# Kernel tuning notes

Hardware: AMD Instinct MI355X
Metric: run time of the kernel (lower is better)

Reference implementation:

```python
import jax, jax.numpy as jnp
import numpy as np

N = 50000
E = 800000
C_IN = 32
C_OUT = 32
K = 8  # number of branch MLPs


def setup_inputs() -> dict:
    key = jax.random.key(0)
    ks = jax.random.split(key, 12)
    x = jax.random.normal(ks[0], (N, C_IN), dtype=jnp.float32)
    pos = jax.random.normal(ks[1], (N, 2), dtype=jnp.float32)
    edge_index = jax.random.randint(ks[2], (2, E), 0, N, dtype=jnp.int32)
    edge_attr = jax.random.normal(ks[3], (E, 4), dtype=jnp.float32)
    edge_weight = jax.random.uniform(ks[4], (E,), dtype=jnp.float32)
    s1 = 1.0 / np.sqrt(C_IN + 4)
    s2 = 1.0 / np.sqrt(C_OUT)
    W1 = jax.random.uniform(ks[5], (K, C_IN + 4, C_OUT), jnp.float32, -s1, s1)
    b1 = jax.random.uniform(ks[6], (K, C_OUT), jnp.float32, -s1, s1)
    W2 = jax.random.uniform(ks[7], (K, C_OUT, C_OUT), jnp.float32, -s2, s2)
    b2 = jax.random.uniform(ks[8], (K, C_OUT), jnp.float32, -s2, s2)
    sr = 1.0 / np.sqrt(C_IN)
    Wr = jax.random.uniform(ks[9], (C_IN, C_OUT), jnp.float32, -sr, sr)
    br = jax.random.uniform(ks[10], (C_OUT,), jnp.float32, -sr, sr)
    return {"x": x, "pos": pos, "edge_index": edge_index, "edge_attr": edge_attr,
            "edge_weight": edge_weight, "W1": W1, "b1": b1, "W2": W2, "b2": b2,
            "Wr": Wr, "br": br}


def reference(x, pos, edge_index, edge_attr, edge_weight, W1, b1, W2, b2, Wr, br):
    src = edge_index[0]  # j (source / neighbor)
    tgt = edge_index[1]  # i (target / aggregation index)

    # gather per-edge features
    x_i = x[tgt]                      # [E, C_IN]
    x_j = x[src]                      # [E, C_IN]
    diff = pos[src] - pos[tgt]        # [E, 2]

    # geometric branch index in [0, 8)
    con0 = (diff[:, 0] > 0).astype(jnp.int32)
    con1 = (diff[:, 1] > 0).astype(jnp.int32)
    con2 = (jnp.abs(diff[:, 0]) - jnp.abs(diff[:, 1]) > 0).astype(jnp.int32)
    idx = con0 + con1 * 2 + con2 * 4  # [E]

    m = jnp.concatenate([x_j - x_i, edge_attr], axis=1)  # [E, C_IN+4]
    # all 8 branch MLPs (Linear->ReLU->Linear->ReLU), then select per edge
    h = jax.nn.relu(jnp.einsum('ec,kcf->ekf', m, W1) + b1[None])   # [E, K, C_OUT]
    f_all = jax.nn.relu(jnp.einsum('ekf,kfg->ekg', h, W2) + b2[None])
    f = jnp.take_along_axis(f_all, idx[:, None, None], axis=1)[:, 0, :]  # [E, C_OUT]
    f = edge_weight[:, None] * f

    # scatter-mean over target nodes
    seg_sum = jax.ops.segment_sum(f, tgt, num_segments=N)
    counts = jax.ops.segment_sum(jnp.ones((f.shape[0],), f.dtype), tgt, num_segments=N)
    out = seg_sum / jnp.maximum(counts, 1.0)[:, None]

    # skip connection
    out = out + x @ Wr + br
    return out
```

## Files before the change

### kernel.cpp

```cpp
#include <hip/hip_runtime.h>

#define N_NODES 50000
#define N_EDGES 800000
#define K_BR    8
#define BCAP    131072
#define MLP_SLOTS (K_BR * BCAP)
#define SCAN_BLOCKS 196
#define BSTRIDE 1024
#define EPT 8
#define P1_BLOCKS 391
#define RB 128
#define RBE 6250


typedef _Float16 h2 __attribute__((ext_vector_type(2)));
typedef _Float16 half8 __attribute__((ext_vector_type(8)));
typedef float f32x4 __attribute__((ext_vector_type(4)));

#define MFMA(a, b, c) __builtin_amdgcn_mfma_f32_16x16x32_f16((a), (b), (c), 0, 0, 0)

#define VAL_MASK 0x3FFFFFFFu
#define FLG_A    0x40000000u
#define FLG_P    0x80000000u


__device__ __forceinline__ int branch_idx(float dx, float dy) {
    return (dx > 0.0f ? 1 : 0) + (dy > 0.0f ? 2 : 0) +
           ((fabsf(dx) - fabsf(dy)) > 0.0f ? 4 : 0);
}

__device__ __forceinline__ unsigned pk_f16pair(float a, float b) {
    h2 p; p.x = (_Float16)a; p.y = (_Float16)b;
    return __builtin_bit_cast(unsigned, p);
}

__device__ __forceinline__ unsigned short f16bits(float a) {
    _Float16 h = (_Float16)a;
    return __builtin_bit_cast(unsigned short, h);
}

__global__ void __launch_bounds__(256) rank_kernel(
    const int* __restrict__ ei, const float* __restrict__ x,
    const float* __restrict__ W1, const float* __restrict__ W2,
    unsigned short* __restrict__ rankB, unsigned short* __restrict__ cntM,
    unsigned* __restrict__ xh, uint4* __restrict__ w1f4, uint4* __restrict__ w2f4) {
    __shared__ unsigned hist[N_NODES / 2];
    int t = threadIdx.x, b = blockIdx.x;
    for (int i = t; i < N_NODES / 2; i += 256) hist[i] = 0;

    int tid = b * 256 + t;
    if (tid < 2048) {
        int L = tid & 63, fl = tid >> 6;
        int nt = fl & 1, kt = (fl >> 1) & 1, k = fl >> 2;
        int quad = L >> 4, col = L & 15;
        unsigned dw[4];
#pragma unroll
        for (int i = 0; i < 4; ++i) {
            float v0 = 0.0f, v1 = 0.0f;
            int k0 = kt * 32 + quad * 8 + 2 * i;
            if (k0 < 36)     v0 = W1[k * 1152 + k0 * 32 + nt * 16 + col];
            if (k0 + 1 < 36) v1 = W1[k * 1152 + (k0 + 1) * 32 + nt * 16 + col];
            dw[i] = pk_f16pair(v0, v1);
        }
        w1f4[tid] = make_uint4(dw[0], dw[1], dw[2], dw[3]);
    } else if (tid < 3072) {
        int u2 = tid - 2048;
        int L = u2 & 63, fl = u2 >> 6;
        int nt = fl & 1, k = fl >> 1;
        int quad = L >> 4, col = L & 15;
        unsigned dw[4];
#pragma unroll
        for (int i = 0; i < 4; ++i) {
            int k0 = quad * 8 + 2 * i;
            dw[i] = pk_f16pair(W2[k * 1024 + k0 * 32 + nt * 16 + col],
                               W2[k * 1024 + (k0 + 1) * 32 + nt * 16 + col]);
        }
        w2f4[u2] = make_uint4(dw[0], dw[1], dw[2], dw[3]);
    }

    __syncthreads();
    int eb = b * RBE;
    for (int it = 0; it < (RBE + 255) / 256; ++it) {
        int r = it * 256 + t;
        if (r < RBE) {
            int e = eb + r;
            int d = ei[N_EDGES + e];
            unsigned add = (d & 1) ? (1u << 16) : 1u;
            unsigned old = atomicAdd(&hist[d >> 1], add);
            unsigned rk = (d & 1) ? (old >> 16) : (old & 0xFFFFu);
            rankB[e] = (unsigned short)rk;
            float2 xv = ((const float2*)x)[e];
            xh[e] = pk_f16pair(xv.x, xv.y);
        }
    }
    __syncthreads();
    unsigned* cm = (unsigned*)(cntM + (size_t)b * N_NODES);
    for (int i = t; i < N_NODES / 2; i += 256) cm[i] = hist[i];
}

__global__ void colscan_kernel(const unsigned short* __restrict__ cntM,
                               unsigned short* __restrict__ blkBase,
                               int* __restrict__ cnt) {
    int d = blockIdx.x * 256 + threadIdx.x;
    if (d >= N_NODES) return;
    int acc = 0;
#pragma unroll 8
    for (int b = 0; b < RB; ++b) {
        size_t i = (size_t)b * N_NODES + d;
        int v = cntM[i];
        blkBase[i] = (unsigned short)acc;
        acc += v;
    }
    cnt[d] = acc;
}

__global__ void pass1_kernel(const int* __restrict__ ei, const float* __restrict__ pos,
                             const float* __restrict__ ea, const float* __restrict__ ew,
                             const unsigned short* __restrict__ rankB,
                             const unsigned short* __restrict__ blkBase,
                             int* __restrict__ bucketCur,
                             uint4* __restrict__ payload) {
    __shared__ int h[K_BR];
    __shared__ int base[K_BR];
    int t = threadIdx.x;
    if (t < K_BR) h[t] = 0;
    __syncthreads();

    int eBase = blockIdx.x * (256 * EPT);
    int sA[EPT], dA[EPT], krA[EPT], slA[EPT];
#pragma unroll
    for (int it = 0; it < EPT; ++it) {
        int e = eBase + it * 256 + t;
        int s = 0, d = 0, k = 0, rank = 0, slot = 0;
        if (e < N_EDGES) {
            s = ei[e]; d = ei[N_EDGES + e];
            float2 ps2 = ((const float2*)pos)[s];
            float2 pd2 = ((const float2*)pos)[d];
            k = branch_idx(ps2.x - pd2.x, ps2.y - pd2.y);
            rank = atomicAdd(&h[k], 1);
            int bb = e / RBE;
            slot = (int)blkBase[(size_t)bb * N_NODES + d] + (int)rankB[e];
        }
        sA[it] = s; dA[it] = d; krA[it] = (k << 16) | rank; slA[it] = slot;
    }
    __syncthreads();
    if (t < K_BR) base[t] = (h[t] > 0) ? atomicAdd(&bucketCur[t * BSTRIDE], h[t]) : 0;
    __syncthreads();
#pragma unroll
    for (int it = 0; it < EPT; ++it) {
        int e = eBase + it * 256 + t;
        if (e < N_EDGES) {
            int k = krA[it] >> 16, rank = krA[it] & 0xFFFF;
            float4 eav = ((const float4*)ea)[e];
            unsigned ewh = (unsigned)f16bits(ew[e]);
            int idx = (k << 17) + base[k] + rank;
            payload[idx] = make_uint4((unsigned)sA[it] | ((unsigned)dA[it] << 16),
                                      (unsigned)slA[it] | (ewh << 16),
                                      pk_f16pair(eav.x, eav.y),
                                      pk_f16pair(eav.z, eav.w));
        }
    }
}

__global__ void scan_kernel(const int* __restrict__ cnt, unsigned* __restrict__ ps,
                            int* __restrict__ nodeStart) {
    __shared__ int s[256];
    __shared__ int sh_off;
    int t = threadIdx.x, b = blockIdx.x;
    int i = b * 256 + t;
    int v = (i < N_NODES) ? cnt[i] : 0;
    s[t] = v;
    __syncthreads();
#pragma unroll
    for (int off = 1; off < 256; off <<= 1) {
        int tmp = (t >= off) ? s[t - off] : 0;
        __syncthreads();
        s[t] += tmp;
        __syncthreads();
    }
    int excl = s[t] - v;
    if (t == 255)
        atomicExch(&ps[b], (unsigned)s[255] | (b == 0 ? FLG_P : FLG_A));
    if (t == 0) sh_off = 0;
    if (t < 64 && b > 0) {
        int off = 0;
        int base = b - 1;
        for (;;) {
            int idx = base - t;
            unsigned w = 0;
            if (idx >= 0) {
                do { w = atomicOr(&ps[idx], 0u); } while (!(w & (FLG_A | FLG_P)));
            }
            bool isP = (w & FLG_P) != 0;
            unsigned long long pm = __ballot(isP);
            int firstP = pm ? (__ffsll((unsigned long long)pm) - 1) : 64;
            int contrib = (idx >= 0 && t <= firstP) ? (int)(w & VAL_MASK) : 0;
#pragma unroll
            for (int sh = 32; sh > 0; sh >>= 1) contrib += __shfl_down(contrib, sh, 64);
            contrib = __shfl(contrib, 0, 64);
            off += contrib;
            if (firstP < 64 || base - 64 < 0) break;
            base -= 64;
        }
        if (t == 0) sh_off = off;
    }
    __syncthreads();
    if (i < N_NODES) nodeStart[i] = excl + sh_off;
}

__global__ void __launch_bounds__(128, 4) mlp_kernel(
    const uint4* __restrict__ payload,
    const unsigned* __restrict__ xh,
    const uint4* __restrict__ w1f4, const float* __restrict__ b1,
    const uint4* __restrict__ w2f4, const float* __restrict__ b2,
    const int* __restrict__ nodeStart,
    const int* __restrict__ bucketFill,
    unsigned short* __restrict__ fbuf) {
    __shared__ uint4 lds4[164];
    char* hreg = (char*)lds4 + (threadIdx.x >> 6) * 1312;

    int t = blockIdx.x * 128 + threadIdx.x;
    int u = __builtin_amdgcn_readfirstlane(t);
    int k = u >> 17;
    int fill = bucketFill[k * BSTRIDE];
    if ((u & (BCAP - 1)) >= fill) return;
    int rel = t & (BCAP - 1);
    bool valid = rel < fill;
    int idx = (k << 17) + min(rel, fill - 1);

    int L = threadIdx.x & 63;
    int quad = L >> 4, col = L & 15;

    uint4 pl = payload[idx];
    int s = (int)(pl.x & 0xFFFFu);
    int d = (int)(pl.x >> 16);
    float whf = (float)__builtin_bit_cast(_Float16, (unsigned short)(pl.y >> 16));
    int slot = valid ? (nodeStart[d] + (int)(pl.y & 0xFFFFu)) : 0;
    int vld = valid ? 1 : 0;

    half8 B1[2][2], B2[2];
#pragma unroll
    for (int kt = 0; kt < 2; ++kt)
#pragma unroll
        for (int nt = 0; nt < 2; ++nt)
            B1[kt][nt] = __builtin_bit_cast(half8, w1f4[((k * 2 + kt) * 2 + nt) * 64 + L]);
#pragma unroll
    for (int nt = 0; nt < 2; ++nt)
        B2[nt] = __builtin_bit_cast(half8, w2f4[(k * 2 + nt) * 64 + L]);
    float b1o0 = b1[k * 32 + col],      b1o1 = b1[k * 32 + 16 + col];
    float b2o0 = b2[k * 32 + col],      b2o1 = b2[k * 32 + 16 + col];

#pragma unroll
    for (int mt = 0; mt < 4; ++mt) {
        int erA = mt * 16 + col;
        int sA = __shfl(s, erA, 64);
        int dAi = __shfl(d, erA, 64);
        unsigned zA = (unsigned)__shfl((int)pl.z, erA, 64);
        unsigned wA = (unsigned)__shfl((int)pl.w, erA, 64);
        uint4 xjv = ((const uint4*)xh)[4 * (size_t)sA + quad];
        uint4 xiv = ((const uint4*)xh)[4 * (size_t)dAi + quad];
        half8 a0 = __builtin_bit_cast(half8, xjv) - __builtin_bit_cast(half8, xiv);
        uint4 a1u = make_uint4(quad == 0 ? zA : 0u, quad == 0 ? wA : 0u, 0u, 0u);
        half8 a1 = __builtin_bit_cast(half8, a1u);

        f32x4 c0 = {b1o0, b1o0, b1o0, b1o0};
        f32x4 c1 = {b1o1, b1o1, b1o1, b1o1};
        c0 = MFMA(a0, B1[0][0], c0);
        c0 = MFMA(a1, B1[1][0], c0);
        c1 = MFMA(a0, B1[0][1], c1);
        c1 = MFMA(a1, B1[1][1], c1);
#pragma unroll
        for (int r = 0; r < 4; ++r) {
            int er = quad * 4 + r;
            *(unsigned short*)(hreg + er * 80 + col * 2)        = f16bits(fmaxf(c0[r], 0.0f));
            *(unsigned short*)(hreg + er * 80 + (16 + col) * 2) = f16bits(fmaxf(c1[r], 0.0f));
        }
        half8 ah = __builtin_bit_cast(half8, *(const uint4*)(hreg + col * 80 + quad * 16));
        f32x4 d0 = {b2o0, b2o0, b2o0, b2o0};
        f32x4 d1 = {b2o1, b2o1, b2o1, b2o1};
        d0 = MFMA(ah, B2[0], d0);
        d1 = MFMA(ah, B2[1], d1);
#pragma unroll
        for (int r = 0; r < 4; ++r) {
            int erC = mt * 16 + quad * 4 + r;
            int slC = __shfl(slot, erC, 64);
            float wC = __shfl(whf, erC, 64);
            int vC = __shfl(vld, erC, 64);
            unsigned short v0 = f16bits(fmaxf(d0[r], 0.0f) * wC);
            unsigned short v1 = f16bits(fmaxf(d1[r], 0.0f) * wC);
            if (vC) {
                unsigned short* orow = fbuf + 32 * (size_t)slC;
                orow[col] = v0;
                orow[16 + col] = v1;
            }
        }
    }
}

__global__ void agg_kernel(const unsigned short* __restrict__ fbuf,
                           const int* __restrict__ nodeStart, const int* __restrict__ deg,
                           const float* __restrict__ x, const float* __restrict__ Wr,
                           const float* __restrict__ br, float* __restrict__ out) {
    int t = blockIdx.x * blockDim.x + threadIdx.x;
    if (t >= N_NODES * 8) return;
    int n = t >> 3, g8 = t & 7;
    int st = nodeStart[n], dg = deg[n];
    const uint2* fb = (const uint2*)fbuf;
    float a0 = 0.0f, a1 = 0.0f, a2 = 0.0f, a3 = 0.0f;
    for (int j = 0; j < dg; ++j) {
        uint2 uu = fb[(size_t)(st + j) * 8 + g8];
        h2 p01 = __builtin_bit_cast(h2, uu.x);
        h2 p23 = __builtin_bit_cast(h2, uu.y);
        a0 += (float)p01.x;
        a1 += (float)p01.y;
        a2 += (float)p23.x;
        a3 += (float)p23.y;
    }
    float inv = 1.0f / (float)max(dg, 1);
    int o = g8 * 4;
    a0 = a0 * inv + br[o];
    a1 = a1 * inv + br[o + 1];
    a2 = a2 * inv + br[o + 2];
    a3 = a3 * inv + br[o + 3];
    const float* xr = x + 32 * (size_t)n;
#pragma unroll
    for (int c = 0; c < 32; ++c) {
        float xv = xr[c];
        a0 = fmaf(xv, Wr[c * 32 + o], a0);
        a1 = fmaf(xv, Wr[c * 32 + o + 1], a1);
        a2 = fmaf(xv, Wr[c * 32 + o + 2], a2);
        a3 = fmaf(xv, Wr[c * 32 + o + 3], a3);
    }
    float4* o4 = (float4*)(out + 32 * (size_t)n + o);
    *o4 = make_float4(a0, a1, a2, a3);
}

extern "C" void kernel_launch(void* const* d_in, const int* in_sizes, int n_in,
                              void* d_out, int out_size, void* d_ws, size_t ws_size,
                              hipStream_t stream) {
    const float* x   = (const float*)d_in[0];
    const float* pos = (const float*)d_in[1];
    const int*   ei  = (const int*)d_in[2];
    const float* ea  = (const float*)d_in[3];
    const float* ew  = (const float*)d_in[4];
    const float* W1  = (const float*)d_in[5];
    const float* b1  = (const float*)d_in[6];
    const float* W2  = (const float*)d_in[7];
    const float* b2  = (const float*)d_in[8];
    const float* Wr  = (const float*)d_in[9];
    const float* br  = (const float*)d_in[10];
    float* out = (float*)d_out;

    char* ws = (char*)d_ws;
    unsigned short* fbuf = (unsigned short*)(ws + 0);
    uint4* payload  = (uint4*)(ws + 51200000);
    int* cnt        = (int*)(ws + 67977216);
    int* bucketCur  = (int*)(ws + 68177216);
    unsigned* psLb  = (unsigned*)(ws + 68209984);
    int* nodeStart  = (int*)(ws + 68210816);
    uint4* w1f4     = (uint4*)(ws + 68410816);
    uint4* w2f4     = (uint4*)(ws + 68443584);
    unsigned* xh    = (unsigned*)(ws + 68459968);
    unsigned short* rankB   = (unsigned short*)(ws + 71659968);
    unsigned short* cntM    = (unsigned short*)(ws + 73259968);
    unsigned short* blkBase = (unsigned short*)(ws + 86059968);

    hipMemsetAsync(bucketCur, 0, 33568, stream);

    rank_kernel<<<RB, 256, 0, stream>>>(ei, x, W1, W2, rankB, cntM, xh, w1f4, w2f4);
    colscan_kernel<<<SCAN_BLOCKS, 256, 0, stream>>>(cntM, blkBase, cnt);
    scan_kernel<<<SCAN_BLOCKS, 256, 0, stream>>>(cnt, psLb, nodeStart);
    pass1_kernel<<<P1_BLOCKS, 256, 0, stream>>>(ei, pos, ea, ew, rankB, blkBase,
                                                bucketCur, payload);
    mlp_kernel<<<MLP_SLOTS / 128, 128, 0, stream>>>(payload, xh, w1f4, b1, w2f4, b2,
                                                    nodeStart, bucketCur, fbuf);
    agg_kernel<<<(N_NODES * 8 + 255) / 256, 256, 0, stream>>>(fbuf, nodeStart, cnt,
                                                              x, Wr, br, out);
}
```

Measured before the change: 189.9 us.

## Pack per-block node histograms into bytes and fuse column scan with prefix scan

The rank kernel now keeps per-block destination counts as 8-bit fields, four nodes per 32-bit LDS word instead of two 16-bit fields, and runs 512 threads per block. This halves shared memory and the cntM matrix written to and read from global memory. The separate column-scan and node prefix-scan kernels are merged into one kernel, which drops a launch and the round trip of cnt through memory. The byte counters can overflow if any node gets more than 255 edges within one 6250-edge block, which is very unlikely for random inputs but not guaranteed.

```diff
diff --git a/kernel.cpp b/kernel.cpp
--- a/kernel.cpp
+++ b/kernel.cpp
@@ -39,16 +39,16 @@
     return __builtin_bit_cast(unsigned short, h);
 }
 
-__global__ void __launch_bounds__(256) rank_kernel(
+__global__ void __launch_bounds__(512) rank_kernel(
     const int* __restrict__ ei, const float* __restrict__ x,
     const float* __restrict__ W1, const float* __restrict__ W2,
-    unsigned short* __restrict__ rankB, unsigned short* __restrict__ cntM,
+    unsigned short* __restrict__ rankB, unsigned char* __restrict__ cntM,
     unsigned* __restrict__ xh, uint4* __restrict__ w1f4, uint4* __restrict__ w2f4) {
-    __shared__ unsigned hist[N_NODES / 2];
+    __shared__ unsigned hist[N_NODES / 4];
     int t = threadIdx.x, b = blockIdx.x;
-    for (int i = t; i < N_NODES / 2; i += 256) hist[i] = 0;
-
-    int tid = b * 256 + t;
+    for (int i = t; i < N_NODES / 4; i += 512) hist[i] = 0;
+
+    int tid = b * 512 + t;
     if (tid < 2048) {
         int L = tid & 63, fl = tid >> 6;
         int nt = fl & 1, kt = (fl >> 1) & 1, k = fl >> 2;
@@ -80,95 +80,43 @@
 
     __syncthreads();
     int eb = b * RBE;
-    for (int it = 0; it < (RBE + 255) / 256; ++it) {
-        int r = it * 256 + t;
+    for (int it = 0; it < (RBE + 511) / 512; ++it) {
+        int r = it * 512 + t;
         if (r < RBE) {
             int e = eb + r;
             int d = ei[N_EDGES + e];
-            unsigned add = (d & 1) ? (1u << 16) : 1u;
-            unsigned old = atomicAdd(&hist[d >> 1], add);
-            unsigned rk = (d & 1) ? (old >> 16) : (old & 0xFFFFu);
-            rankB[e] = (unsigned short)rk;
+            unsigned sh = (unsigned)(d & 3) * 8u;
+            unsigned old = atomicAdd(&hist[d >> 2], 1u << sh);
+            rankB[e] = (unsigned short)((old >> sh) & 0xFFu);
             float2 xv = ((const float2*)x)[e];
             xh[e] = pk_f16pair(xv.x, xv.y);
         }
     }
     __syncthreads();
     unsigned* cm = (unsigned*)(cntM + (size_t)b * N_NODES);
-    for (int i = t; i < N_NODES / 2; i += 256) cm[i] = hist[i];
-}
-
-__global__ void colscan_kernel(const unsigned short* __restrict__ cntM,
-                               unsigned short* __restrict__ blkBase,
-                               int* __restrict__ cnt) {
-    int d = blockIdx.x * 256 + threadIdx.x;
-    if (d >= N_NODES) return;
-    int acc = 0;
-#pragma unroll 8
-    for (int b = 0; b < RB; ++b) {
-        size_t i = (size_t)b * N_NODES + d;
-        int v = cntM[i];
-        blkBase[i] = (unsigned short)acc;
-        acc += v;
-    }
-    cnt[d] = acc;
-}
-
-__global__ void pass1_kernel(const int* __restrict__ ei, const float* __restrict__ pos,
-                             const float* __restrict__ ea, const float* __restrict__ ew,
-                             const unsigned short* __restrict__ rankB,
-                             const unsigned short* __restrict__ blkBase,
-                             int* __restrict__ bucketCur,
-                             uint4* __restrict__ payload) {
-    __shared__ int h[K_BR];
-    __shared__ int base[K_BR];
-    int t = threadIdx.x;
-    if (t < K_BR) h[t] = 0;
-    __syncthreads();
-
-    int eBase = blockIdx.x * (256 * EPT);
-    int sA[EPT], dA[EPT], krA[EPT], slA[EPT];
-#pragma unroll
-    for (int it = 0; it < EPT; ++it) {
-        int e = eBase + it * 256 + t;
-        int s = 0, d = 0, k = 0, rank = 0, slot = 0;
-        if (e < N_EDGES) {
-            s = ei[e]; d = ei[N_EDGES + e];
-            float2 ps2 = ((const float2*)pos)[s];
-            float2 pd2 = ((const float2*)pos)[d];
-            k = branch_idx(ps2.x - pd2.x, ps2.y - pd2.y);
-            rank = atomicAdd(&h[k], 1);
-            int bb = e / RBE;
-            slot = (int)blkBase[(size_t)bb * N_NODES + d] + (int)rankB[e];
-        }
-        sA[it] = s; dA[it] = d; krA[it] = (k << 16) | rank; slA[it] = slot;
-    }
-    __syncthreads();
-    if (t < K_BR) base[t] = (h[t] > 0) ? atomicAdd(&bucketCur[t * BSTRIDE], h[t]) : 0;
-    __syncthreads();
-#pragma unroll
-    for (int it = 0; it < EPT; ++it) {
-        int e = eBase + it * 256 + t;
-        if (e < N_EDGES) {
-            int k = krA[it] >> 16, rank = krA[it] & 0xFFFF;
-            float4 eav = ((const float4*)ea)[e];
-            unsigned ewh = (unsigned)f16bits(ew[e]);
-            int idx = (k << 17) + base[k] + rank;
-            payload[idx] = make_uint4((unsigned)sA[it] | ((unsigned)dA[it] << 16),
-                                      (unsigned)slA[it] | (ewh << 16),
-                                      pk_f16pair(eav.x, eav.y),
-                                      pk_f16pair(eav.z, eav.w));
-        }
-    }
-}
-
-__global__ void scan_kernel(const int* __restrict__ cnt, unsigned* __restrict__ ps,
-                            int* __restrict__ nodeStart) {
+    for (int i = t; i < N_NODES / 4; i += 512) cm[i] = hist[i];
+}
+
+__global__ void cscan_kernel(const unsigned char* __restrict__ cntM,
+                             unsigned short* __restrict__ blkBase,
+                             int* __restrict__ cnt, unsigned* __restrict__ ps,
+                             int* __restrict__ nodeStart) {
     __shared__ int s[256];
     __shared__ int sh_off;
     int t = threadIdx.x, b = blockIdx.x;
-    int i = b * 256 + t;
-    int v = (i < N_NODES) ? cnt[i] : 0;
+    int d = b * 256 + t;
+    int acc = 0;
+    if (d < N_NODES) {
+#pragma unroll 8
+        for (int blk = 0; blk < RB; ++blk) {
+            size_t i = (size_t)blk * N_NODES + d;
+            int v = cntM[i];
+            blkBase[i] = (unsigned short)acc;
+            acc += v;
+        }
+        cnt[d] = acc;
+    }
+    int v = (d < N_NODES) ? acc : 0;
     s[t] = v;
     __syncthreads();
 #pragma unroll
@@ -205,7 +153,55 @@
         if (t == 0) sh_off = off;
     }
     __syncthreads();
-    if (i < N_NODES) nodeStart[i] = excl + sh_off;
+    if (d < N_NODES) nodeStart[d] = excl + sh_off;
+}
+
+__global__ void pass1_kernel(const int* __restrict__ ei, const float* __restrict__ pos,
+                             const float* __restrict__ ea, const float* __restrict__ ew,
+                             const unsigned short* __restrict__ rankB,
+                             const unsigned short* __restrict__ blkBase,
+                             int* __restrict__ bucketCur,
+                             uint4* __restrict__ payload) {
+    __shared__ int h[K_BR];
+    __shared__ int base[K_BR];
+    int t = threadIdx.x;
+    if (t < K_BR) h[t] = 0;
+    __syncthreads();
+
+    int eBase = blockIdx.x * (256 * EPT);
+    int sA[EPT], dA[EPT], krA[EPT], slA[EPT];
+#pragma unroll
+    for (int it = 0; it < EPT; ++it) {
+        int e = eBase + it * 256 + t;
+        int s = 0, d = 0, k = 0, rank = 0, slot = 0;
+        if (e < N_EDGES) {
+            s = ei[e]; d = ei[N_EDGES + e];
+            float2 ps2 = ((const float2*)pos)[s];
+            float2 pd2 = ((const float2*)pos)[d];
+            k = branch_idx(ps2.x - pd2.x, ps2.y - pd2.y);
+            rank = atomicAdd(&h[k], 1);
+            int bb = e / RBE;
+            slot = (int)blkBase[(size_t)bb * N_NODES + d] + (int)rankB[e];
+        }
+        sA[it] = s; dA[it] = d; krA[it] = (k << 16) | rank; slA[it] = slot;
+    }
+    __syncthreads();
+    if (t < K_BR) base[t] = (h[t] > 0) ? atomicAdd(&bucketCur[t * BSTRIDE], h[t]) : 0;
+    __syncthreads();
+#pragma unroll
+    for (int it = 0; it < EPT; ++it) {
+        int e = eBase + it * 256 + t;
+        if (e < N_EDGES) {
+            int k = krA[it] >> 16, rank = krA[it] & 0xFFFF;
+            float4 eav = ((const float4*)ea)[e];
+            unsigned ewh = (unsigned)f16bits(ew[e]);
+            int idx = (k << 17) + base[k] + rank;
+            payload[idx] = make_uint4((unsigned)sA[it] | ((unsigned)dA[it] << 16),
+                                      (unsigned)slA[it] | (ewh << 16),
+                                      pk_f16pair(eav.x, eav.y),
+                                      pk_f16pair(eav.z, eav.w));
+        }
+    }
 }
 
 __global__ void __launch_bounds__(128, 4) mlp_kernel(
@@ -361,15 +357,14 @@
     uint4* w1f4     = (uint4*)(ws + 68410816);
     uint4* w2f4     = (uint4*)(ws + 68443584);
     unsigned* xh    = (unsigned*)(ws + 68459968);
-    unsigned short* rankB   = (unsigned short*)(ws + 71659968);
-    unsigned short* cntM    = (unsigned short*)(ws + 73259968);
+    unsigned short* rankB = (unsigned short*)(ws + 71659968);
+    unsigned char* cntM   = (unsigned char*)(ws + 73259968);
     unsigned short* blkBase = (unsigned short*)(ws + 86059968);
 
     hipMemsetAsync(bucketCur, 0, 33568, stream);
 
-    rank_kernel<<<RB, 256, 0, stream>>>(ei, x, W1, W2, rankB, cntM, xh, w1f4, w2f4);
-    colscan_kernel<<<SCAN_BLOCKS, 256, 0, stream>>>(cntM, blkBase, cnt);
-    scan_kernel<<<SCAN_BLOCKS, 256, 0, stream>>>(cnt, psLb, nodeStart);
+    rank_kernel<<<RB, 512, 0, stream>>>(ei, x, W1, W2, rankB, cntM, xh, w1f4, w2f4);
+    cscan_kernel<<<SCAN_BLOCKS, 256, 0, stream>>>(cntM, blkBase, cnt, psLb, nodeStart);
     pass1_kernel<<<P1_BLOCKS, 256, 0, stream>>>(ei, pos, ea, ew, rankB, blkBase,
                                                 bucketCur, payload);
     mlp_kernel<<<MLP_SLOTS / 128, 128, 0, stream>>>(payload, xh, w1f4, b1, w2f4, b2,
```

New measurement: 185.6 us. -2.2%, faster.
